# Performance work log

Measured on AMD Instinct MI355X. Metric: run time of the kernel, lower is better.

The kernel has to match this reference:

```python
import jax, jax.numpy as jnp
import numpy as np

B, C, U, V, H, W = 4, 64, 5, 5, 64, 64
MID = 64  # mid_dim defaults to dim


def setup_inputs() -> dict:
    key = jax.random.key(0)
    ks = jax.random.split(key, 13)
    s = 0.05
    inp = {"x": jax.random.normal(ks[0], (B, C, U, V, H, W), dtype=jnp.float32)}
    # body: Conv2d(dim->mid,1x1), SiLU, Conv2d(mid->dim,1x1)
    inp["w1"] = jax.random.normal(ks[1], (MID, C), dtype=jnp.float32) * s
    inp["b1"] = jax.random.normal(ks[2], (MID,), dtype=jnp.float32) * s
    inp["w2"] = jax.random.normal(ks[3], (C, MID), dtype=jnp.float32) * s
    inp["b2"] = jax.random.normal(ks[4], (C,), dtype=jnp.float32) * s
    # four fuse 1x1 convs (dim->dim)
    for i in range(4):
        inp[f"fw{i}"] = jax.random.normal(ks[5 + 2 * i], (C, C), dtype=jnp.float32) * s
        inp[f"fb{i}"] = jax.random.normal(ks[6 + 2 * i], (C,), dtype=jnp.float32) * s
    return inp


def _conv1x1(w, b, x):
    # x: (B,C,h,w); w: (O,C); 1x1 conv == channel matmul
    return jnp.einsum('oc,bchw->bohw', w, x) + b[None, :, None, None]


def reference(x, w1, b1, w2, b2, fw0, fb0, fw1, fb1, fw2, fb2, fw3, fb3):
    # Four 2-axis mean pools over the 6D tensor
    hw_m = x.mean(axis=(2, 3))   # (B,C,H,W)
    uv_m = x.mean(axis=(4, 5))   # (B,C,U,V)
    uh_m = x.mean(axis=(3, 5))   # (B,C,U,H)
    vw_m = x.mean(axis=(2, 4))   # (B,C,V,W)
    # Assemble padded buffer uvhw of shape (B,C,H+V,W+U)
    top = jnp.concatenate([hw_m, jnp.swapaxes(uh_m, -1, -2)], axis=-1)  # (B,C,H,W+U)
    bot = jnp.concatenate([vw_m, jnp.swapaxes(uv_m, -1, -2)], axis=-1)  # (B,C,V,W+U)
    uvhw = jnpp_concat = jnp.concatenate([top, bot], axis=-2)           # (B,C,H+V,W+U)
    # body: conv1x1 -> SiLU -> conv1x1
    uvhw = _conv1x1(w2, b2, jax.nn.silu(_conv1x1(w1, b1, uvhw)))
    # Split back into the four pooled maps
    hw = uvhw[..., :H, :W]
    vw = uvhw[..., H:, :W]
    uh = jnp.swapaxes(uvhw[..., :H, W:], -1, -2)  # (B,C,U,H)
    uv = jnp.swapaxes(uvhw[..., H:, W:], -1, -2)  # (B,C,U,V)
    # Per-branch fuse convs, then broadcast-gate x and sum
    hw = _conv1x1(fw0, fb0, hw).reshape(B, C, 1, 1, H, W)
    uv = _conv1x1(fw1, fb1, uv).reshape(B, C, U, V, 1, 1)
    uh = _conv1x1(fw2, fb2, uh).reshape(B, C, U, 1, H, 1)
    vw = _conv1x1(fw3, fb3, vw).reshape(B, C, 1, V, 1, W)
    return x * hw + x * uv + x * uh + x * vw
```

## Files before the change

### kernel.cpp

```cpp
#include <hip/hip_runtime.h>
#include <hip/hip_bf16.h>
#include <cstddef>

#define BB 4
#define CC 64
#define UU 5
#define VV 5
#define HH 64
#define WW 64
#define NIJ (69*69)

typedef float f4v __attribute__((ext_vector_type(4)));

__device__ __forceinline__ float rdlane(float v, int l) {
    return __uint_as_float((unsigned)__builtin_amdgcn_readlane((int)__float_as_uint(v), l));
}
__device__ __forceinline__ float rfl(float v) {
    return __uint_as_float((unsigned)__builtin_amdgcn_readfirstlane((int)__float_as_uint(v)));
}
__device__ __forceinline__ float sum4(float4 a) { return (a.x+a.y)+(a.z+a.w); }
__device__ __forceinline__ void nt_store4(float4 r, float4* p) {
    union { float4 s; f4v v; } u; u.s = r;
    __builtin_nontemporal_store(u.v, (f4v*)p);
}

__global__ __launch_bounds__(512) void k1_means(const float* __restrict__ x,
        float* __restrict__ m_hw, float* __restrict__ R,
        float* __restrict__ vw_part) {
    const int bid  = blockIdx.x;
    const int bc   = bid >> 1;
    const int half = bid & 1;
    const int t    = threadIdx.x;
    const int p    = half*512 + t;
    const int wave = t >> 6;
    const int lane = t & 63;

    const float4* xt = (const float4*)x + (size_t)bc * 25600;

    __shared__ float smem[25*512];

    float4 hw = make_float4(0.f,0.f,0.f,0.f);
    float4 vwacc[5];
    #pragma unroll
    for (int v = 0; v < 5; ++v) vwacc[v] = make_float4(0.f,0.f,0.f,0.f);

    #pragma unroll
    for (int u = 0; u < 5; ++u) {
        #pragma unroll
        for (int v = 0; v < 5; ++v) {
            float4 q = xt[(u*5 + v)*1024 + p];
            hw.x += q.x; hw.y += q.y; hw.z += q.z; hw.w += q.w;
            vwacc[v].x += q.x; vwacc[v].y += q.y;
            vwacc[v].z += q.z; vwacc[v].w += q.w;
            smem[(u*5 + v)*512 + t] = sum4(q);
        }
    }

    float4 o;
    o.x = hw.x*(1.f/25.f); o.y = hw.y*(1.f/25.f);
    o.z = hw.z*(1.f/25.f); o.w = hw.w*(1.f/25.f);
    ((float4*)m_hw)[(size_t)bc*1024 + p] = o;

    __syncthreads();

    for (int task = t; task < 800; task += 512) {
        const int k    = task >> 5;
        const int hloc = task & 31;
        const float* row = &smem[k*512 + hloc*16];
        float s = 0.f;
        #pragma unroll
        for (int j = 0; j < 16; ++j) s += row[j];
        R[((size_t)bc*25 + k)*64 + half*32 + hloc] = s;
    }
    __syncthreads();

    float4* vwbuf = (float4*)smem;
    #pragma unroll
    for (int v = 0; v < 5; ++v) {
        float4 s = vwacc[v];
        s.x += __shfl_xor(s.x, 16); s.y += __shfl_xor(s.y, 16);
        s.z += __shfl_xor(s.z, 16); s.w += __shfl_xor(s.w, 16);
        s.x += __shfl_xor(s.x, 32); s.y += __shfl_xor(s.y, 32);
        s.z += __shfl_xor(s.z, 32); s.w += __shfl_xor(s.w, 32);
        if (lane < 16) vwbuf[(wave*5 + v)*16 + lane] = s;
    }
    __syncthreads();

    if (t < 80) {
        const int v = t >> 4;
        float4 s = vwbuf[(0*5 + v)*16 + (t & 15)];
        #pragma unroll
        for (int w8 = 1; w8 < 8; ++w8) {
            float4 pp = vwbuf[(w8*5 + v)*16 + (t & 15)];
            s.x += pp.x; s.y += pp.y; s.z += pp.z; s.w += pp.w;
        }
        ((float4*)vw_part)[(size_t)bid*80 + t] = s;
    }
}

__global__ __launch_bounds__(256) void k1b_assemble(
        const float* __restrict__ m_hw, const float* __restrict__ R,
        const float* __restrict__ vw_part, float* __restrict__ grid_t) {
    __shared__ float tile[64][68];
    const int blk = blockIdx.x;
    const bool top = blk < 256;
    const int t = threadIdx.x;
    const int c = t >> 2;
    const int qs = t & 3;

    int b, i;
    if (top) {
        b = blk >> 6;
        const int h = blk & 63;
        i = h;
        #pragma unroll
        for (int j = 0; j < 4; ++j) {
            const int q = 4*j + qs;
            float4 v = ((const float4*)m_hw)[((size_t)(b*64 + c))*1024 + h*16 + q];
            const int w = q * 4;
            tile[w+0][c] = v.x; tile[w+1][c] = v.y;
            tile[w+2][c] = v.z; tile[w+3][c] = v.w;
        }
        for (int idx = t; idx < 320; idx += 256) {
            const int u = idx >> 6, cc = idx & 63;
            const float* Rp = R + (((size_t)(b*64 + cc)*25) + u*5)*64 + h;
            float s = Rp[0] + Rp[64] + Rp[128] + Rp[192] + Rp[256];
            grid_t[((size_t)b*NIJ + h*69 + 64 + u)*64 + cc] = s * (1.f/320.f);
        }
    } else {
        b = (blk - 256) / 5;
        const int v = (blk - 256) % 5;
        i = 64 + v;
        #pragma unroll
        for (int j = 0; j < 4; ++j) {
            const int wq = 4*j + qs;
            float4 p0 = ((const float4*)vw_part)[((size_t)(b*64 + c)*2 + 0)*80 + v*16 + wq];
            float4 p1 = ((const float4*)vw_part)[((size_t)(b*64 + c)*2 + 1)*80 + v*16 + wq];
            const int w = wq * 4;
            const float sc = 1.f/320.f;
            tile[w+0][c] = (p0.x + p1.x)*sc; tile[w+1][c] = (p0.y + p1.y)*sc;
            tile[w+2][c] = (p0.z + p1.z)*sc; tile[w+3][c] = (p0.w + p1.w)*sc;
        }
        for (int idx = t; idx < 320; idx += 256) {
            const int u = idx >> 6, cc = idx & 63;
            const float4* Rp4 = (const float4*)(R + (((size_t)(b*64 + cc)*25) + u*5 + v)*64);
            float4 a = make_float4(0.f,0.f,0.f,0.f);
            #pragma unroll
            for (int k = 0; k < 16; ++k) {
                float4 pp = Rp4[k];
                a.x += pp.x; a.y += pp.y; a.z += pp.z; a.w += pp.w;
            }
            grid_t[((size_t)b*NIJ + i*69 + 64 + u)*64 + cc] = sum4(a) * (1.f/4096.f);
        }
    }
    __syncthreads();

    float4* dst4 = (float4*)grid_t + ((size_t)b*NIJ + i*69) * 16;
    #pragma unroll
    for (int k = 0; k < 4; ++k) {
        const int oidx = k*256 + t;
        const int w = oidx >> 4, cq = (oidx & 15) * 4;
        float4 v;
        v.x = tile[w][cq]; v.y = tile[w][cq+1];
        v.z = tile[w][cq+2]; v.w = tile[w][cq+3];
        dst4[oidx] = v;
    }
}

#define LOADROW(dst, src)                                              \
    { _Pragma("unroll")                                                \
      for (int q = 0; q < 16; ++q) {                                   \
          float4 t4 = ((const float4*)(src))[lane*16 + q];             \
          dst[4*q+0] = t4.x; dst[4*q+1] = t4.y;                        \
          dst[4*q+2] = t4.z; dst[4*q+3] = t4.w;                        \
      } }

#define DOT64(res, wr, src)                                            \
    float res;                                                         \
    { float _a0=0.f,_a1=0.f,_a2=0.f,_a3=0.f;                           \
      _Pragma("unroll")                                                \
      for (int cc2 = 0; cc2 < 64; cc2 += 4) {                          \
          _a0 = fmaf(wr[cc2+0], rdlane(src, cc2+0), _a0);              \
          _a1 = fmaf(wr[cc2+1], rdlane(src, cc2+1), _a1);              \
          _a2 = fmaf(wr[cc2+2], rdlane(src, cc2+2), _a2);              \
          _a3 = fmaf(wr[cc2+3], rdlane(src, cc2+3), _a3);              \
      }                                                                \
      res = (_a0 + _a1) + (_a2 + _a3); }

#define MLP_BODY(J)                                                    \
    {                                                                  \
        const int jj = (J);                                            \
        float v = gtb[(size_t)(i*69 + jj) * CC + lane];                \
        DOT64(d1, w1r, v);                                             \
        float acc1 = d1 + b1v;                                         \
        float ya = acc1 / (1.f + __expf(-acc1));                       \
        DOT64(d2, w2r, ya);                                            \
        float acc2 = d2 + b2v;                                         \
        DOT64(d3, fr, acc2);                                           \
        sp[(size_t)(jj - jbase) * sstr] = d3 + fbv;                    \
    }

__global__ __launch_bounds__(64, 1) void k2_mlp(
        const float* __restrict__ grid_t,
        const float* __restrict__ w1, const float* __restrict__ b1,
        const float* __restrict__ w2, const float* __restrict__ b2,
        const float* __restrict__ fw0, const float* __restrict__ fb0,
        const float* __restrict__ fw1, const float* __restrict__ fb1,
        const float* __restrict__ fw2, const float* __restrict__ fb2,
        const float* __restrict__ fw3, const float* __restrict__ fb3,
        float* __restrict__ mod_hw, float* __restrict__ mod_uh,
        float* __restrict__ mod_vw, float* __restrict__ mod_uv) {
    const int blk  = blockIdx.x;
    const int row  = blk >> 2;
    const int chnk = blk & 3;
    const int b    = row / 69;
    const int i    = row % 69;
    const int lane = threadIdx.x & 63;

    const int j0 = chnk * 18;
    const int j1 = min(69, j0 + 18);
    const bool top = (i < 64);

    const float* fwA = top ? fw0 : fw3;
    const float* fbA = top ? fb0 : fb3;
    const float* fwB = top ? fw2 : fw1;
    const float* fbB = top ? fb2 : fb1;

    float w1r[64], w2r[64], fr[64];
    LOADROW(w1r, w1);
    LOADROW(w2r, w2);
    const float b1v = b1[lane];
    const float b2v = b2[lane];

    const float* gtb = grid_t + (size_t)b * NIJ * CC;
    const int cbl = b * CC + lane;

    const int jm = min(j1, 64);
    if (j0 < jm) {
        LOADROW(fr, fwA);
        const float fbv = fbA[lane];
        float* sp; int sstr; const int jbase = 0;
        if (top) { sp = mod_hw + ((size_t)cbl*64 + i)*64;          sstr = 1; }
        else     { sp = mod_vw + (size_t)cbl*320 + (i-64)*64;      sstr = 1; }
        for (int j = j0; j < jm; ++j) MLP_BODY(j)
    }
    if (j1 > 64) {
        LOADROW(fr, fwB);
        const float fbv = fbB[lane];
        float* sp; int sstr; const int jbase = 64;
        if (top) { sp = mod_uh + (size_t)cbl*320 + i;              sstr = 64; }
        else     { sp = mod_uv + (size_t)cbl*25 + (i-64);          sstr = 5;  }
        const int jb = max(j0, 64);
        for (int j = jb; j < j1; ++j) MLP_BODY(j)
    }
}

__global__ __launch_bounds__(256, 4) void k3_apply(
        const float* __restrict__ x,
        const float* __restrict__ mod_hw, const float* __restrict__ mod_uh,
        const float* __restrict__ mod_vw, const float* __restrict__ mod_uv,
        float* __restrict__ out) {
    const int blk  = blockIdx.x;
    const int bc   = blk >> 2;
    const int qt   = blk & 3;
    const int t    = threadIdx.x;
    const int base = qt*256 + t;
    const int h    = base >> 4;

    float4 mh = ((const float4*)(mod_hw + (size_t)bc * 4096))[base];
    float uh[5];
    #pragma unroll
    for (int u = 0; u < 5; ++u) uh[u] = mod_uh[(size_t)bc*320 + u*64 + h];
    float4 vw[5];
    #pragma unroll
    for (int v = 0; v < 5; ++v)
        vw[v] = ((const float4*)(mod_vw + (size_t)bc*320 + v*64))[t & 15];
    float uv[25];
    #pragma unroll
    for (int k = 0; k < 25; ++k)
        uv[k] = rfl(mod_uv[(size_t)bc*25 + k]);

    const float4* x4 = (const float4*)(x + (size_t)bc * (UU*VV*HH*WW));
    float4* o4 = (float4*)(out + (size_t)bc * (UU*VV*HH*WW));

    #pragma unroll
    for (int u = 0; u < 5; ++u) {
        #pragma unroll
        for (int v = 0; v < 5; ++v) {
            const int idx = (u*5 + v)*1024 + base;
            float4 xv = x4[idx];
            const float s = uh[u] + uv[u*5 + v];
            float4 r;
            r.x = xv.x * (mh.x + vw[v].x + s);
            r.y = xv.y * (mh.y + vw[v].y + s);
            r.z = xv.z * (mh.z + vw[v].z + s);
            r.w = xv.w * (mh.w + vw[v].w + s);
            nt_store4(r, &o4[idx]);
        }
    }
}

extern "C" void kernel_launch(void* const* d_in, const int* in_sizes, int n_in,
                              void* d_out, int out_size, void* d_ws, size_t ws_size,
                              hipStream_t stream) {
    const float* x   = (const float*)d_in[0];
    const float* w1  = (const float*)d_in[1];
    const float* b1  = (const float*)d_in[2];
    const float* w2  = (const float*)d_in[3];
    const float* b2  = (const float*)d_in[4];
    const float* fw0 = (const float*)d_in[5];
    const float* fb0 = (const float*)d_in[6];
    const float* fw1 = (const float*)d_in[7];
    const float* fb1 = (const float*)d_in[8];
    const float* fw2 = (const float*)d_in[9];
    const float* fb2 = (const float*)d_in[10];
    const float* fw3 = (const float*)d_in[11];
    const float* fb3 = (const float*)d_in[12];

    float* ws = (float*)d_ws;
    float* grid_t = ws;
    float* mod_hw = ws + 1218816;
    float* mod_uh = mod_hw + 1048576;
    float* mod_vw = mod_uh + 81920;
    float* mod_uv = mod_vw + 81920;

    float* m_hw    = (float*)d_out;
    float* Rbuf    = m_hw + 1048576;
    float* vw_part = Rbuf + 409600;

    k1_means<<<BB*CC*2, 512, 0, stream>>>(x, m_hw, Rbuf, vw_part);
    k1b_assemble<<<BB*CC + BB*VV, 256, 0, stream>>>(m_hw, Rbuf, vw_part, grid_t);
    k2_mlp<<<BB*69*4, 64, 0, stream>>>(grid_t, w1, b1, w2, b2,
                                       fw0, fb0, fw1, fb1, fw2, fb2, fw3, fb3,
                                       mod_hw, mod_uh, mod_vw, mod_uv);
    k3_apply<<<BB*CC*4, 256, 0, stream>>>(x, mod_hw, mod_uh, mod_vw, mod_uv,
                                          (float*)d_out);
}
```

Before: 108.0 us.

## Fuse grid assembly into MLP kernel, reading pooled means directly

Removes the separate assemble kernel that transposed pooled means into a channel-last grid buffer. The MLP kernel now reads each lane's channel value straight from the pooled mean buffers and the partial sums, finishing the uh/uv reductions inline. This saves one launch and a full write and read of the intermediate grid. The cost is strided, uncoalesced per-lane loads, since each lane now reads a different channel plane, plus redundant reduction work inside the MLP loop.

```diff
diff --git a/kernel.cpp b/kernel.cpp
--- a/kernel.cpp
+++ b/kernel.cpp
@@ -8,7 +8,6 @@
 #define VV 5
 #define HH 64
 #define WW 64
-#define NIJ (69*69)
 
 typedef float f4v __attribute__((ext_vector_type(4)));
 
@@ -95,75 +94,6 @@
             s.x += pp.x; s.y += pp.y; s.z += pp.z; s.w += pp.w;
         }
         ((float4*)vw_part)[(size_t)bid*80 + t] = s;
-    }
-}
-
-__global__ __launch_bounds__(256) void k1b_assemble(
-        const float* __restrict__ m_hw, const float* __restrict__ R,
-        const float* __restrict__ vw_part, float* __restrict__ grid_t) {
-    __shared__ float tile[64][68];
-    const int blk = blockIdx.x;
-    const bool top = blk < 256;
-    const int t = threadIdx.x;
-    const int c = t >> 2;
-    const int qs = t & 3;
-
-    int b, i;
-    if (top) {
-        b = blk >> 6;
-        const int h = blk & 63;
-        i = h;
-        #pragma unroll
-        for (int j = 0; j < 4; ++j) {
-            const int q = 4*j + qs;
-            float4 v = ((const float4*)m_hw)[((size_t)(b*64 + c))*1024 + h*16 + q];
-            const int w = q * 4;
-            tile[w+0][c] = v.x; tile[w+1][c] = v.y;
-            tile[w+2][c] = v.z; tile[w+3][c] = v.w;
-        }
-        for (int idx = t; idx < 320; idx += 256) {
-            const int u = idx >> 6, cc = idx & 63;
-            const float* Rp = R + (((size_t)(b*64 + cc)*25) + u*5)*64 + h;
-            float s = Rp[0] + Rp[64] + Rp[128] + Rp[192] + Rp[256];
-            grid_t[((size_t)b*NIJ + h*69 + 64 + u)*64 + cc] = s * (1.f/320.f);
-        }
-    } else {
-        b = (blk - 256) / 5;
-        const int v = (blk - 256) % 5;
-        i = 64 + v;
-        #pragma unroll
-        for (int j = 0; j < 4; ++j) {
-            const int wq = 4*j + qs;
-            float4 p0 = ((const float4*)vw_part)[((size_t)(b*64 + c)*2 + 0)*80 + v*16 + wq];
-            float4 p1 = ((const float4*)vw_part)[((size_t)(b*64 + c)*2 + 1)*80 + v*16 + wq];
-            const int w = wq * 4;
-            const float sc = 1.f/320.f;
-            tile[w+0][c] = (p0.x + p1.x)*sc; tile[w+1][c] = (p0.y + p1.y)*sc;
-            tile[w+2][c] = (p0.z + p1.z)*sc; tile[w+3][c] = (p0.w + p1.w)*sc;
-        }
-        for (int idx = t; idx < 320; idx += 256) {
-            const int u = idx >> 6, cc = idx & 63;
-            const float4* Rp4 = (const float4*)(R + (((size_t)(b*64 + cc)*25) + u*5 + v)*64);
-            float4 a = make_float4(0.f,0.f,0.f,0.f);
-            #pragma unroll
-            for (int k = 0; k < 16; ++k) {
-                float4 pp = Rp4[k];
-                a.x += pp.x; a.y += pp.y; a.z += pp.z; a.w += pp.w;
-            }
-            grid_t[((size_t)b*NIJ + i*69 + 64 + u)*64 + cc] = sum4(a) * (1.f/4096.f);
-        }
-    }
-    __syncthreads();
-
-    float4* dst4 = (float4*)grid_t + ((size_t)b*NIJ + i*69) * 16;
-    #pragma unroll
-    for (int k = 0; k < 4; ++k) {
-        const int oidx = k*256 + t;
-        const int w = oidx >> 4, cq = (oidx & 15) * 4;
-        float4 v;
-        v.x = tile[w][cq]; v.y = tile[w][cq+1];
-        v.z = tile[w][cq+2]; v.w = tile[w][cq+3];
-        dst4[oidx] = v;
     }
 }
 
@@ -187,21 +117,21 @@
       }                                                                \
       res = (_a0 + _a1) + (_a2 + _a3); }
 
-#define MLP_BODY(J)                                                    \
+#define MLP_CORE(VIN, OUTEXPR)                                         \
     {                                                                  \
-        const int jj = (J);                                            \
-        float v = gtb[(size_t)(i*69 + jj) * CC + lane];                \
+        float v = (VIN);                                               \
         DOT64(d1, w1r, v);                                             \
         float acc1 = d1 + b1v;                                         \
         float ya = acc1 / (1.f + __expf(-acc1));                       \
         DOT64(d2, w2r, ya);                                            \
         float acc2 = d2 + b2v;                                         \
         DOT64(d3, fr, acc2);                                           \
-        sp[(size_t)(jj - jbase) * sstr] = d3 + fbv;                    \
+        OUTEXPR = d3 + fbv;                                            \
     }
 
 __global__ __launch_bounds__(64, 1) void k2_mlp(
-        const float* __restrict__ grid_t,
+        const float* __restrict__ m_hw, const float* __restrict__ R,
+        const float* __restrict__ vw_part,
         const float* __restrict__ w1, const float* __restrict__ b1,
         const float* __restrict__ w2, const float* __restrict__ b2,
         const float* __restrict__ fw0, const float* __restrict__ fb0,
@@ -232,26 +162,56 @@
     const float b1v = b1[lane];
     const float b2v = b2[lane];
 
-    const float* gtb = grid_t + (size_t)b * NIJ * CC;
-    const int cbl = b * CC + lane;
+    const int b64c = b * CC + lane;
+    const int cbl  = b64c;
 
     const int jm = min(j1, 64);
     if (j0 < jm) {
         LOADROW(fr, fwA);
         const float fbv = fbA[lane];
-        float* sp; int sstr; const int jbase = 0;
-        if (top) { sp = mod_hw + ((size_t)cbl*64 + i)*64;          sstr = 1; }
-        else     { sp = mod_vw + (size_t)cbl*320 + (i-64)*64;      sstr = 1; }
-        for (int j = j0; j < jm; ++j) MLP_BODY(j)
+        if (top) {
+            const float* src = m_hw + (size_t)b64c*4096 + i*64;
+            float* sp = mod_hw + ((size_t)cbl*64 + i)*64;
+            for (int j = j0; j < jm; ++j)
+                MLP_CORE(src[j], sp[j])
+        } else {
+            const float* p0 = vw_part + (size_t)b64c*640 + (i-64)*64;
+            const float* q0 = vw_part + ((size_t)b64c*2 + 0)*320 + (i-64)*64;
+            const float* q1 = vw_part + ((size_t)b64c*2 + 1)*320 + (i-64)*64;
+            float* sp = mod_vw + (size_t)cbl*320 + (i-64)*64;
+            (void)p0;
+            for (int j = j0; j < jm; ++j)
+                MLP_CORE((q0[j] + q1[j]) * (1.f/320.f), sp[j])
+        }
     }
     if (j1 > 64) {
         LOADROW(fr, fwB);
         const float fbv = fbB[lane];
-        float* sp; int sstr; const int jbase = 64;
-        if (top) { sp = mod_uh + (size_t)cbl*320 + i;              sstr = 64; }
-        else     { sp = mod_uv + (size_t)cbl*25 + (i-64);          sstr = 5;  }
         const int jb = max(j0, 64);
-        for (int j = jb; j < j1; ++j) MLP_BODY(j)
+        if (top) {
+            float* sp = mod_uh + (size_t)cbl*320 + i;
+            for (int j = jb; j < j1; ++j) {
+                const int u = j - 64;
+                const float* Rp = R + ((size_t)b64c*25 + u*5)*64 + i;
+                float vin = (Rp[0] + Rp[64] + Rp[128] + Rp[192] + Rp[256])
+                            * (1.f/320.f);
+                MLP_CORE(vin, sp[(size_t)u*64])
+            }
+        } else {
+            float* sp = mod_uv + (size_t)cbl*25 + (i-64);
+            for (int j = jb; j < j1; ++j) {
+                const int u = j - 64;
+                const float4* Rp4 = (const float4*)(R
+                    + ((size_t)b64c*25 + u*5 + (i-64))*64);
+                float4 a = make_float4(0.f,0.f,0.f,0.f);
+                #pragma unroll
+                for (int k = 0; k < 16; ++k) {
+                    float4 pp = Rp4[k];
+                    a.x += pp.x; a.y += pp.y; a.z += pp.z; a.w += pp.w;
+                }
+                MLP_CORE(sum4(a) * (1.f/4096.f), sp[(size_t)u*5])
+            }
+        }
     }
 }
 
@@ -318,8 +278,7 @@
     const float* fb3 = (const float*)d_in[12];
 
     float* ws = (float*)d_ws;
-    float* grid_t = ws;
-    float* mod_hw = ws + 1218816;
+    float* mod_hw = ws;
     float* mod_uh = mod_hw + 1048576;
     float* mod_vw = mod_uh + 81920;
     float* mod_uv = mod_vw + 81920;
@@ -329,8 +288,7 @@
     float* vw_part = Rbuf + 409600;
 
     k1_means<<<BB*CC*2, 512, 0, stream>>>(x, m_hw, Rbuf, vw_part);
-    k1b_assemble<<<BB*CC + BB*VV, 256, 0, stream>>>(m_hw, Rbuf, vw_part, grid_t);
-    k2_mlp<<<BB*69*4, 64, 0, stream>>>(grid_t, w1, b1, w2, b2,
+    k2_mlp<<<BB*69*4, 64, 0, stream>>>(m_hw, Rbuf, vw_part, w1, b1, w2, b2,
                                        fw0, fb0, fw1, fb1, fw2, fb2, fw3, fb3,
                                        mod_hw, mod_uh, mod_vw, mod_uv);
     k3_apply<<<BB*CC*4, 256, 0, stream>>>(x, mod_hw, mod_uh, mod_vw, mod_uv,
```

New measurement: 100.4 us. -7.0%, faster.
